# Kernel optimization log

Hardware: AMD Instinct MI355X
Metric: run time of the kernel (lower is better)

Reference implementation:

```python
import jax, jax.numpy as jnp
import numpy as np

ALPHA = 0.1       # args.alpha
T = 1.0           # args.T temperature
SIGMA = 64.0      # Gaussian kernel bandwidth of kernel_function
B_CONST = 1.0     # B in get_lambda
N_ITERS = 50      # 2^-50 << tol=1e-8, matches the break condition of the 1000-iter loop
HW = 256          # image resolution (upsample target)


def _features(feat):
    # get_feature: bilinear upsample (align_corners=False == half-pixel, as jax.image.resize) then sigmoid(x/T)
    n, c, _, _ = feat.shape
    up = jax.image.resize(feat, (n, c, HW, HW), method='bilinear')
    return jax.nn.sigmoid(up / T)


def setup_inputs() -> dict:
    key = jax.random.key(0)
    k1, k2, k3, k4 = jax.random.split(key, 4)
    return {
        'cal_feat': jax.random.normal(k1, (256, 1, 64, 64), jnp.float32),
        'test_feat': jax.random.normal(k2, (32, 1, 64, 64), jnp.float32),
        'cal_gt': jax.random.randint(k3, (256, 1, 256, 256), 0, 2, jnp.int32),
        'test_gt': jax.random.randint(k4, (32, 1, 256, 256), 0, 2, jnp.int32),
    }


def reference(cal_feat, test_feat, cal_gt, test_gt):
    cal_res = _features(cal_feat)    # [N,1,H,W] in (0,1)
    test_res = _features(test_feat)  # [B,1,H,W]
    N = cal_res.shape[0]
    B = test_res.shape[0]
    f32 = cal_res.dtype

    # kernel_function.get_weight: Gaussian RBF on flattened features, plus self-weight 1, row-normalized -> [B, N+1]
    cf = cal_res.reshape(N, -1)
    tf = test_res.reshape(B, -1)
    d2 = (tf * tf).sum(-1)[:, None] + (cf * cf).sum(-1)[None, :] - 2.0 * (tf @ cf.T)
    k = jnp.exp(-d2 / (2.0 * SIGMA * SIGMA))
    w = jnp.concatenate([k, jnp.ones((B, 1), f32)], axis=1)
    w = w / w.sum(axis=1, keepdims=True)

    # FNR_i(t) = #{positive pixels of cal sample i with score < t} / #positives
    # (pred = res >= t, so false negatives are positive pixels with res < t). Precompute sorted
    # positive-pixel scores per cal sample so the bisection is a batched searchsorted.
    gt = (cal_gt > 0).reshape(N, -1)
    pos = jnp.sum(gt, axis=1)                                    # [N]
    scores = jnp.where(gt, cal_res.reshape(N, -1), jnp.inf)
    sorted_scores = jnp.sort(scores, axis=1)                     # [N, HW*HW], padding at +inf
    pos_f = jnp.maximum(pos, 1).astype(f32)

    def fnr_at(t):  # t: [B] thresholds -> [N, B]
        cnt = jax.vmap(lambda s: jnp.searchsorted(s, t, side='left'))(sorted_scores)
        return cnt.astype(f32) / pos_f[:, None]

    # batched bisection on lambda (get_lambda, vectorized over the B test samples)
    def body(carry, _):
        low, high = carry
        lam = 0.5 * (low + high)
        fnr = fnr_at(1.0 - lam)                                   # [N, B]
        risk = jnp.einsum('bn,nb->b', w[:, :-1], fnr) + w[:, -1] * B_CONST
        high = jnp.where(risk < ALPHA, lam, high)
        low = jnp.where(risk >= ALPHA, lam, low)
        return (low, high), None

    init = (jnp.zeros((B,), f32), jnp.ones((B,), f32))
    (low, _), _ = jax.lax.scan(body, init, None, length=N_ITERS)
    lam = low  # _lambda = low after the loop

    # prediction set, size and per-test FNR (get_fnr_list on the test sample)
    pred = test_res >= (1.0 - lam)[:, None, None, None]           # [B,1,H,W] bool
    size = jnp.sum(pred, axis=(1, 2, 3)).astype(f32)
    tgt = test_gt > 0
    tp = jnp.sum(pred & tgt, axis=(1, 2, 3)).astype(f32)
    tpos = jnp.maximum(jnp.sum(tgt, axis=(1, 2, 3)), 1).astype(f32)
    fnr_test = 1.0 - tp / tpos                                    # fdr_tensor, [B]
    return fnr_test, lam, size
```

## Files before the change

### kernel.cpp

```cpp
#include <hip/hip_runtime.h>


#define NPIX 65536
#define HB 16256
#define CDF_STRIDE 16272
#define ALPHA 0.1f

#define OFF_TESTRES  0
#define OFF_CALBF    8388608u
#define OFF_TESTBF   41943040u
#define OFF_GROUPED  46137344u
#define OFF_CDF      79691776u
#define OFF_GPART    96354304u
#define OFF_CC       98451456u
#define OFF_THR      98452480u
#define OFF_LAM      98452608u
#define OFF_FACC     98452736u

typedef __attribute__((ext_vector_type(8))) short bf16x8;
typedef __attribute__((ext_vector_type(16))) float f32x16;

__device__ __forceinline__ unsigned short f2bf_rne(float f) {
  unsigned u = __float_as_uint(f);
  return (unsigned short)((u + 0x7FFFu + ((u >> 16) & 1u)) >> 16);
}

struct RowIp {
  const float* f;
  int x0, x1;
  float omwx, wx;
  __device__ __forceinline__ float operator()(int j) const {
    return f[j * 64 + x0] * omwx + f[j * 64 + x1] * wx;
  }
};

template<int MCNT, typename RV, typename BODY>
__device__ __forceinline__ void scan_rows(RV rv, bool lowq, float omwy, float wy,
                                          int m0, BODY body) {
  if (lowq) {
    float rP = rv(m0 > 0 ? m0 - 1 : 0);
    #pragma unroll 8
    for (int i = 0; i < MCNT; ++i) {
      float rC = rv(m0 + i);
      float v = rP * omwy + rC * wy;
      body(i, 1.f / (1.f + __expf(-v)));
      rP = rC;
    }
  } else {
    float rC = rv(m0);
    #pragma unroll 8
    for (int i = 0; i < MCNT; ++i) {
      int j = m0 + i + 1;
      if (j > 63) j = 63;
      float rN = rv(j);
      float v = rC * omwy + rN * wy;
      body(i, 1.f / (1.f + __expf(-v)));
      rC = rN;
    }
  }
}

__global__ __launch_bounds__(1024, 4) void k_cal(const float* __restrict__ featc,
                                                 const int* __restrict__ gt,
                                                 unsigned short* __restrict__ calbf,
                                                 unsigned* __restrict__ cdf,
                                                 unsigned short* __restrict__ grouped,
                                                 float* __restrict__ cc,
                                                 const float* __restrict__ featt,
                                                 float* __restrict__ tres,
                                                 unsigned short* __restrict__ tbf) {
  __shared__ unsigned smem[16384];
  __shared__ float ri[16384];
  const int n = blockIdx.x, tid = threadIdx.x;
  const int lane = tid & 63, wv = tid >> 6;
  const int x = tid & 255, yq = tid >> 8;
  for (int i = tid; i < 16320; i += 1024) smem[i] = 0;
  const float* fc = featc + n * 4096;
  for (int flat = tid; flat < 16384; flat += 1024) {
    int m = flat >> 8, xx = flat & 255;
    float sxx = 0.25f * (float)xx - 0.375f;
    int x0f = (int)floorf(sxx);
    float wxx = sxx - (float)x0f;
    int xx1 = x0f + 1;
    int xx0 = x0f < 0 ? 0 : x0f;
    if (xx1 > 63) xx1 = 63;
    ri[flat] = fc[m * 64 + xx0] * (1.f - wxx) + fc[m * 64 + xx1] * wxx;
  }
  const int* gtn = gt + (size_t)n * NPIX;
  unsigned short* cbn = calbf + (size_t)n * NPIX;
  float sx = 0.25f * (float)x - 0.375f;
  int x0 = (int)floorf(sx);
  float wx = sx - (float)x0;
  int x1 = x0 + 1;
  if (x0 < 0) x0 = 0;
  if (x1 > 63) x1 = 63;
  const float wy = (yq == 0) ? 0.625f : (yq == 1) ? 0.875f : (yq == 2) ? 0.125f : 0.375f;
  const float omwy = 1.f - wy;
  const bool lowq = (yq < 2);
  const int pb = (yq << 8) + x;
  __syncthreads();
  const float* rix = ri + x;
  auto rv = [&](int j) { return rix[j << 8]; };
  unsigned long long pm = 0ull;
  float sumsq = 0.f;
  scan_rows<64>(rv, lowq, omwy, wy, 0, [&](int i, float s) {
    int p = (i << 10) + pb;
    unsigned short bh = f2bf_rne(s);
    cbn[p] = bh;
    float sr = __uint_as_float((unsigned)bh << 16);
    sumsq += sr * sr;
    if (gtn[p] > 0) {
      pm |= (1ull << i);
      atomicAdd(&smem[__float_as_uint(s) >> 16], 1u);
    }
  });
  #pragma unroll
  for (int off = 32; off; off >>= 1) sumsq += __shfl_xor(sumsq, off);
  if (lane == 0) smem[16336 + wv] = __float_as_uint(sumsq);
  __syncthreads();
  if (tid == 0) {
    float c = 0.f;
    for (int w = 0; w < 16; ++w) c += __uint_as_float(smem[16336 + w]);
    cc[n] = c;
  }
  unsigned* cdfn = cdf + (size_t)n * CDF_STRIDE;
  if (tid < 256) {
    const int base = tid * 64;
    unsigned psum = 0;
    if (base < HB) {
      for (int j = 0; j < 64; ++j) psum += smem[base + ((j + tid) & 63)];
    }
    unsigned inc = psum;
    #pragma unroll
    for (int off = 1; off < 64; off <<= 1) {
      unsigned v = __shfl_up(inc, off);
      if (lane >= off) inc += v;
    }
    if (lane == 63) smem[16320 + wv] = inc;
  }
  __syncthreads();
  if (tid < 256) {
    const int base = tid * 64;
    unsigned psum = 0;
    if (base < HB) {
      for (int j = 0; j < 64; ++j) psum += smem[base + ((j + tid) & 63)];
    }
    unsigned inc = psum;
    #pragma unroll
    for (int off = 1; off < 64; off <<= 1) {
      unsigned v = __shfl_up(inc, off);
      if (lane >= off) inc += v;
    }
    unsigned woff = 0;
    for (int w = 0; w < wv; ++w) woff += smem[16320 + w];
    unsigned run = woff + inc - psum;
    if (base < HB) {
      for (int j = 0; j < 64; ++j) {
        unsigned h = smem[base + j];
        smem[base + j] = run;
        run += h;
      }
    }
    if (tid == 255) cdfn[HB] = woff + inc;
  }
  __syncthreads();
  for (int i = tid; i < HB; i += 1024) cdfn[i] = smem[i];
  __syncthreads();
  unsigned short* gn = grouped + (size_t)n * NPIX;
  scan_rows<64>(rv, lowq, omwy, wy, 0, [&](int i, float s) {
    if (pm & (1ull << i)) {
      unsigned bits = __float_as_uint(s);
      unsigned idx = atomicAdd(&smem[bits >> 16], 1u);
      gn[idx] = (unsigned short)(bits & 0xFFFFu);
    }
  });
  const int tb2 = n >> 3, m0 = (n & 7) * 8;
  const float* tfp = featt + tb2 * 4096;
  float* resb = tres + (size_t)tb2 * NPIX;
  unsigned short* tbn = tbf + (size_t)tb2 * NPIX;
  const RowIp rvt{tfp, x0, x1, 1.f - wx, wx};
  const int pbt = ((m0 * 4 + yq) << 8) + x;
  scan_rows<8>(rvt, lowq, omwy, wy, m0, [&](int i, float s) {
    int p = pbt + (i << 10);
    resb[p] = s;
    tbn[p] = f2bf_rne(s);
  });
}

__global__ __launch_bounds__(256) void k_gemm(const unsigned short* __restrict__ tbf,
                                              const unsigned short* __restrict__ cbf,
                                              float* __restrict__ gpart) {
  __shared__ __align__(16) unsigned short As[16384];
  __shared__ __align__(16) unsigned short Bs[16384];
  __shared__ float lred[4][1024];
  const int tid = threadIdx.x;
  const int lane = tid & 63, wv = tid >> 6;
  const int r = lane & 31, half = lane >> 5;
  const int nt = blockIdx.x;
  f32x16 acc;
  #pragma unroll
  for (int i = 0; i < 16; ++i) acc[i] = 0.f;
  for (int ch = 0; ch < 2; ++ch) {
    const size_t kbase = (size_t)blockIdx.y * 1024 + ch * 512;
    __syncthreads();
    #pragma unroll
    for (int s = 0; s < 16; ++s) {
      int flat = s * 256 + tid;
      int rem = flat & 2047;
      int row = rem >> 6, kb = rem & 63;
      const unsigned short* src = (flat >= 2048)
          ? cbf + (size_t)(nt * 32 + row) * NPIX + kbase + kb * 8
          : tbf + (size_t)row * NPIX + kbase + kb * 8;
      int slot = ((kb << 5) + row) ^ (kb & 31);
      int4 v = *(const int4*)src;
      *(int4*)((flat >= 2048 ? Bs : As) + slot * 8) = v;
    }
    __syncthreads();
    #pragma unroll
    for (int i = 0; i < 8; ++i) {
      int k8 = (wv << 4) + i * 2 + half;
      int slot = ((k8 << 5) + r) ^ (k8 & 31);
      bf16x8 a = *(const bf16x8*)(As + slot * 8);
      bf16x8 b = *(const bf16x8*)(Bs + slot * 8);
      acc = __builtin_amdgcn_mfma_f32_32x32x16_bf16(a, b, acc, 0, 0, 0);
    }
  }
  #pragma unroll
  for (int rg = 0; rg < 16; ++rg) {
    int m = (rg & 3) + 8 * (rg >> 2) + 4 * half;
    lred[wv][m * 32 + r] = acc[rg];
  }
  __syncthreads();
  float* gp = gpart + (size_t)(blockIdx.y * 8 + nt) * 1024;
  for (int e = tid; e < 1024; e += 256)
    gp[e] = lred[0][e] + lred[1][e] + lred[2][e] + lred[3][e];
}

__global__ __launch_bounds__(512) void k_quant(const float* __restrict__ gpart,
                                               const float* __restrict__ cc,
                                               const unsigned* __restrict__ cdf,
                                               const unsigned short* __restrict__ grouped,
                                               const unsigned short* __restrict__ tbf,
                                               float* __restrict__ lam,
                                               float* __restrict__ thr,
                                               int* __restrict__ facc) {
  __shared__ float qs[256];
  __shared__ float bins[4096];
  __shared__ float red[8];
  __shared__ float bc[4];
  __shared__ unsigned sBin;
  const int b = blockIdx.x, tid = threadIdx.x;
  const int lane = tid & 63, wv = tid >> 6;

  if (tid < 4) facc[b * 4 + tid] = 0;
  for (int i = tid; i < 4096; i += 512) bins[i] = 0.f;
  if (tid == 0) sBin = 0xFFFFFFFFu;

  float ts = 0.f;
  const int4* tbp = (const int4*)(tbf + (size_t)b * NPIX);
  for (int i = tid; i < 8192; i += 512) {
    int4 v = tbp[i];
    unsigned w0 = (unsigned)v.x, w1 = (unsigned)v.y, w2 = (unsigned)v.z, w3 = (unsigned)v.w;
    float f;
    f = __uint_as_float(w0 << 16); ts += f * f;
    f = __uint_as_float(w0 & 0xFFFF0000u); ts += f * f;
    f = __uint_as_float(w1 << 16); ts += f * f;
    f = __uint_as_float(w1 & 0xFFFF0000u); ts += f * f;
    f = __uint_as_float(w2 << 16); ts += f * f;
    f = __uint_as_float(w2 & 0xFFFF0000u); ts += f * f;
    f = __uint_as_float(w3 << 16); ts += f * f;
    f = __uint_as_float(w3 & 0xFFFF0000u); ts += f * f;
  }
  #pragma unroll
  for (int off = 32; off; off >>= 1) ts += __shfl_xor(ts, off);
  if (lane == 0) red[wv] = ts;
  __syncthreads();
  if (tid == 0) {
    float t = 0.f;
    for (int w = 0; w < 8; ++w) t += red[w];
    bc[0] = t;
  }
  __syncthreads();
  const float ttv = bc[0];

  float k = 0.f;
  if (tid < 256) {
    const float* gp = gpart + ((tid >> 5) * 1024) + (b * 32) + (tid & 31);
    float g = 0.f;
    #pragma unroll 8
    for (int ks = 0; ks < 64; ++ks) g += gp[(size_t)ks * 8192];
    float d2 = ttv + cc[tid] - 2.f * g;
    k = expf(-d2 * (1.f / 8192.f));
  }
  float v = k;
  #pragma unroll
  for (int off = 32; off; off >>= 1) v += __shfl_xor(v, off);
  if (lane == 0) red[wv] = v;
  __syncthreads();
  if (tid == 0) {
    float ws = 1.f;
    for (int w = 0; w < 8; ++w) ws += red[w];
    bc[1] = ws;
  }
  __syncthreads();
  const float wsum = bc[1];
  const float wlast = 1.f / wsum;
  const float R = ALPHA - wlast;
  if (R <= 0.f) {
    if (tid == 0) { lam[b] = 1.0f; thr[b] = 0.0f; }
    return;
  }
  if (tid < 256) {
    unsigned pos = cdf[(size_t)tid * CDF_STRIDE + HB];
    qs[tid] = k / (wsum * (float)(pos ? pos : 1u));
  }
  __syncthreads();

  int lo = 0, hi = HB;
  float baseS = 0.f;
  for (int it = 0; it < 14; ++it) {
    int mid = (lo + hi) >> 1;
    float p = 0.f;
    if (tid < 256) p = qs[tid] * (float)cdf[(size_t)tid * CDF_STRIDE + mid];
    float r = p;
    #pragma unroll
    for (int off = 32; off; off >>= 1) r += __shfl_xor(r, off);
    if (lane == 0) red[wv] = r;
    __syncthreads();
    if (tid == 0) {
      float s = 0.f;
      for (int w = 0; w < 8; ++w) s += red[w];
      bc[2] = s;
    }
    __syncthreads();
    float S = bc[2];
    if (S < R) { lo = mid; baseS = S; } else { hi = mid; }
  }
  const int B = lo;

  {
    const int n = tid >> 1;
    const float q = qs[n];
    const unsigned* cn = cdf + (size_t)n * CDF_STRIDE;
    const unsigned short* gn = grouped + (size_t)n * NPIX;
    unsigned e0 = cn[B + 1];
    for (unsigned j = cn[B] + (tid & 1); j < e0; j += 2)
      atomicAdd(&bins[gn[j] >> 4], q);
  }
  __syncthreads();

  if (wv == 0) {
    float s = 0.f;
    for (int j = 0; j < 64; ++j) s += bins[lane * 64 + j];
    float inc = s;
    #pragma unroll
    for (int off = 1; off < 64; off <<= 1) {
      float u = __shfl_up(inc, off);
      if (lane >= off) inc += u;
    }
    float pre = inc - s;
    bool hit = (baseS + pre < R) && (baseS + inc >= R);
    unsigned long long m = __ballot(hit);
    int ow = m ? (__ffsll((unsigned long long)m) - 1) : -1;
    if (lane == ow) {
      float run = baseS + pre;
      unsigned bin = (unsigned)lane * 64 + 63;
      for (int j = 0; j < 64; ++j) {
        float bv = bins[lane * 64 + j];
        if (run + bv >= R) { bin = (unsigned)lane * 64 + j; break; }
        run += bv;
      }
      sBin = bin;
    }
    if (m == 0 && lane == 0) sBin = 4095u;
  }
  __syncthreads();
  if (tid == 0) {
    unsigned tb = ((unsigned)B << 16) | (sBin << 4);
    lam[b] = 1.0f - __uint_as_float(tb | 0x8u);
    thr[b] = __uint_as_float((tb | 0xFu) + 1u);
  }
}

__global__ __launch_bounds__(256) void k_finalp(const float* __restrict__ tres,
                                                const int* __restrict__ tgt,
                                                const float* __restrict__ thr,
                                                const float* __restrict__ lam,
                                                int* __restrict__ facc,
                                                float* __restrict__ out) {
  __shared__ int red[12];
  const int b = blockIdx.x, seg = blockIdx.y, tid = threadIdx.x;
  const int lane = tid & 63, wv = tid >> 6;
  const float th = thr[b];
  const float* rb = tres + (size_t)b * NPIX + seg * 8192;
  const int* gb = tgt + (size_t)b * NPIX + seg * 8192;
  int sz = 0, tp = 0, tpos = 0;
  for (int i = 0; i < 32; ++i) {
    int p = i * 256 + tid;
    int pred = (rb[p] >= th) ? 1 : 0;
    int tg = (gb[p] > 0) ? 1 : 0;
    sz += pred;
    tp += pred & tg;
    tpos += tg;
  }
  #pragma unroll
  for (int off = 32; off; off >>= 1) {
    sz += __shfl_xor(sz, off);
    tp += __shfl_xor(tp, off);
    tpos += __shfl_xor(tpos, off);
  }
  if (lane == 0) { red[wv] = sz; red[4 + wv] = tp; red[8 + wv] = tpos; }
  __syncthreads();
  if (tid == 0) {
    int s0 = red[0] + red[1] + red[2] + red[3];
    int s1 = red[4] + red[5] + red[6] + red[7];
    int s2 = red[8] + red[9] + red[10] + red[11];
    atomicAdd(&facc[b * 4 + 0], s0);
    atomicAdd(&facc[b * 4 + 1], s1);
    atomicAdd(&facc[b * 4 + 2], s2);
    __threadfence();
    int old = atomicAdd(&facc[b * 4 + 3], 1);
    if (old == 7) {
      int fsz = atomicAdd(&facc[b * 4 + 0], 0);
      int ftp = atomicAdd(&facc[b * 4 + 1], 0);
      int ftpos = atomicAdd(&facc[b * 4 + 2], 0);
      float tposf = (float)(ftpos > 0 ? ftpos : 1);
      out[b] = 1.f - (float)ftp / tposf;
      out[32 + b] = lam[b];
      out[64 + b] = (float)fsz;
    }
  }
}

extern "C" void kernel_launch(void* const* d_in, const int* in_sizes, int n_in,
                              void* d_out, int out_size, void* d_ws, size_t ws_size,
                              hipStream_t stream) {
  const float* cal_feat = (const float*)d_in[0];
  const float* test_feat = (const float*)d_in[1];
  const int* cal_gt = (const int*)d_in[2];
  const int* test_gt = (const int*)d_in[3];
  float* out = (float*)d_out;
  char* ws = (char*)d_ws;

  float* test_res = (float*)(ws + OFF_TESTRES);
  unsigned short* cal_bf = (unsigned short*)(ws + OFF_CALBF);
  unsigned short* test_bf = (unsigned short*)(ws + OFF_TESTBF);
  unsigned short* grouped = (unsigned short*)(ws + OFF_GROUPED);
  unsigned* cdf = (unsigned*)(ws + OFF_CDF);
  float* gpart = (float*)(ws + OFF_GPART);
  float* cc = (float*)(ws + OFF_CC);
  float* thr = (float*)(ws + OFF_THR);
  float* lam = (float*)(ws + OFF_LAM);
  int* facc = (int*)(ws + OFF_FACC);

  k_cal<<<dim3(256), dim3(1024), 0, stream>>>(cal_feat, cal_gt, cal_bf, cdf, grouped, cc,
                                              test_feat, test_res, test_bf);
  k_gemm<<<dim3(8, 64), dim3(256), 0, stream>>>(test_bf, cal_bf, gpart);
  k_quant<<<dim3(32), dim3(512), 0, stream>>>(gpart, cc, cdf, grouped, test_bf, lam, thr, facc);
  k_finalp<<<dim3(32, 8), dim3(256), 0, stream>>>(test_res, test_gt, thr, lam, facc, out);
}
```

Baseline: 251.2 us.

## Fuse final prediction-set reduction into quantile kernel and vectorize bin scatter

New measurement: 254.4 us. No clear change (+1.3%).

```diff
diff --git a/kernel.cpp b/kernel.cpp
--- a/kernel.cpp
+++ b/kernel.cpp
@@ -13,9 +13,6 @@
 #define OFF_CDF      79691776u
 #define OFF_GPART    96354304u
 #define OFF_CC       98451456u
-#define OFF_THR      98452480u
-#define OFF_LAM      98452608u
-#define OFF_FACC     98452736u
 
 typedef __attribute__((ext_vector_type(8))) short bf16x8;
 typedef __attribute__((ext_vector_type(16))) float f32x16;
@@ -241,18 +238,18 @@
                                                const unsigned* __restrict__ cdf,
                                                const unsigned short* __restrict__ grouped,
                                                const unsigned short* __restrict__ tbf,
-                                               float* __restrict__ lam,
-                                               float* __restrict__ thr,
-                                               int* __restrict__ facc) {
+                                               const float* __restrict__ tres,
+                                               const int* __restrict__ tgt,
+                                               float* __restrict__ out) {
   __shared__ float qs[256];
   __shared__ float bins[4096];
   __shared__ float red[8];
   __shared__ float bc[4];
   __shared__ unsigned sBin;
+  __shared__ int ired[24];
   const int b = blockIdx.x, tid = threadIdx.x;
   const int lane = tid & 63, wv = tid >> 6;
 
-  if (tid < 4) facc[b * 4 + tid] = 0;
   for (int i = tid; i < 4096; i += 512) bins[i] = 0.f;
   if (tid == 0) sBin = 0xFFFFFFFFu;
 
@@ -300,108 +297,113 @@
   if (tid == 0) {
     float ws = 1.f;
     for (int w = 0; w < 8; ++w) ws += red[w];
-    bc[1] = ws;
-  }
-  __syncthreads();
-  const float wsum = bc[1];
-  const float wlast = 1.f / wsum;
-  const float R = ALPHA - wlast;
-  if (R <= 0.f) {
-    if (tid == 0) { lam[b] = 1.0f; thr[b] = 0.0f; }
-    return;
-  }
-  if (tid < 256) {
-    unsigned pos = cdf[(size_t)tid * CDF_STRIDE + HB];
-    qs[tid] = k / (wsum * (float)(pos ? pos : 1u));
-  }
-  __syncthreads();
-
-  int lo = 0, hi = HB;
-  float baseS = 0.f;
-  for (int it = 0; it < 14; ++it) {
-    int mid = (lo + hi) >> 1;
-    float p = 0.f;
-    if (tid < 256) p = qs[tid] * (float)cdf[(size_t)tid * CDF_STRIDE + mid];
-    float r = p;
-    #pragma unroll
-    for (int off = 32; off; off >>= 1) r += __shfl_xor(r, off);
-    if (lane == 0) red[wv] = r;
+    bc[0] = ws;
+  }
+  __syncthreads();
+  const float wsum = bc[0];
+  const float R = ALPHA - 1.f / wsum;
+
+  if (R > 0.f) {
+    if (tid < 256) {
+      unsigned pos = cdf[(size_t)tid * CDF_STRIDE + HB];
+      qs[tid] = k / (wsum * (float)(pos ? pos : 1u));
+    }
+    __syncthreads();
+    int lo = 0, hi = HB;
+    float baseS = 0.f;
+    for (int it = 0; it < 14; ++it) {
+      int mid = (lo + hi) >> 1;
+      float p = 0.f;
+      if (tid < 256) p = qs[tid] * (float)cdf[(size_t)tid * CDF_STRIDE + mid];
+      float r = p;
+      #pragma unroll
+      for (int off = 32; off; off >>= 1) r += __shfl_xor(r, off);
+      if (lane == 0) red[wv] = r;
+      __syncthreads();
+      if (tid == 0) {
+        float s = 0.f;
+        for (int w = 0; w < 8; ++w) s += red[w];
+        bc[1] = s;
+      }
+      __syncthreads();
+      float S = bc[1];
+      if (S < R) { lo = mid; baseS = S; } else { hi = mid; }
+    }
+    const int B = lo;
+
+    {
+      const int n = tid >> 1;
+      const float q = qs[n];
+      const unsigned* cn = cdf + (size_t)n * CDF_STRIDE;
+      const unsigned short* gn = grouped + (size_t)n * NPIX;
+      unsigned s0 = cn[B], e0 = cn[B + 1];
+      unsigned mid = (s0 + e0) >> 1;
+      unsigned a0 = (tid & 1) ? mid : s0;
+      unsigned a1 = (tid & 1) ? e0 : mid;
+      while (a0 < a1 && (a0 & 7u)) { atomicAdd(&bins[gn[a0] >> 4], q); ++a0; }
+      for (; a0 + 8 <= a1; a0 += 8) {
+        int4 vv = *(const int4*)(gn + a0);
+        unsigned u0 = (unsigned)vv.x, u1 = (unsigned)vv.y, u2 = (unsigned)vv.z, u3 = (unsigned)vv.w;
+        atomicAdd(&bins[(u0 & 0xFFFFu) >> 4], q);
+        atomicAdd(&bins[u0 >> 20], q);
+        atomicAdd(&bins[(u1 & 0xFFFFu) >> 4], q);
+        atomicAdd(&bins[u1 >> 20], q);
+        atomicAdd(&bins[(u2 & 0xFFFFu) >> 4], q);
+        atomicAdd(&bins[u2 >> 20], q);
+        atomicAdd(&bins[(u3 & 0xFFFFu) >> 4], q);
+        atomicAdd(&bins[u3 >> 20], q);
+      }
+      for (; a0 < a1; ++a0) atomicAdd(&bins[gn[a0] >> 4], q);
+    }
+    __syncthreads();
+
+    if (wv == 0) {
+      float s = 0.f;
+      for (int j = 0; j < 64; ++j) s += bins[lane * 64 + j];
+      float inc = s;
+      #pragma unroll
+      for (int off = 1; off < 64; off <<= 1) {
+        float u = __shfl_up(inc, off);
+        if (lane >= off) inc += u;
+      }
+      float pre = inc - s;
+      bool hit = (baseS + pre < R) && (baseS + inc >= R);
+      unsigned long long m = __ballot(hit);
+      int ow = m ? (__ffsll((unsigned long long)m) - 1) : -1;
+      if (lane == ow) {
+        float run = baseS + pre;
+        unsigned bin = (unsigned)lane * 64 + 63;
+        for (int j = 0; j < 64; ++j) {
+          float bv = bins[lane * 64 + j];
+          if (run + bv >= R) { bin = (unsigned)lane * 64 + j; break; }
+          run += bv;
+        }
+        sBin = bin;
+      }
+      if (m == 0 && lane == 0) sBin = 4095u;
+    }
     __syncthreads();
     if (tid == 0) {
-      float s = 0.f;
-      for (int w = 0; w < 8; ++w) s += red[w];
-      bc[2] = s;
-    }
-    __syncthreads();
-    float S = bc[2];
-    if (S < R) { lo = mid; baseS = S; } else { hi = mid; }
-  }
-  const int B = lo;
-
-  {
-    const int n = tid >> 1;
-    const float q = qs[n];
-    const unsigned* cn = cdf + (size_t)n * CDF_STRIDE;
-    const unsigned short* gn = grouped + (size_t)n * NPIX;
-    unsigned e0 = cn[B + 1];
-    for (unsigned j = cn[B] + (tid & 1); j < e0; j += 2)
-      atomicAdd(&bins[gn[j] >> 4], q);
-  }
-  __syncthreads();
-
-  if (wv == 0) {
-    float s = 0.f;
-    for (int j = 0; j < 64; ++j) s += bins[lane * 64 + j];
-    float inc = s;
-    #pragma unroll
-    for (int off = 1; off < 64; off <<= 1) {
-      float u = __shfl_up(inc, off);
-      if (lane >= off) inc += u;
-    }
-    float pre = inc - s;
-    bool hit = (baseS + pre < R) && (baseS + inc >= R);
-    unsigned long long m = __ballot(hit);
-    int ow = m ? (__ffsll((unsigned long long)m) - 1) : -1;
-    if (lane == ow) {
-      float run = baseS + pre;
-      unsigned bin = (unsigned)lane * 64 + 63;
-      for (int j = 0; j < 64; ++j) {
-        float bv = bins[lane * 64 + j];
-        if (run + bv >= R) { bin = (unsigned)lane * 64 + j; break; }
-        run += bv;
-      }
-      sBin = bin;
-    }
-    if (m == 0 && lane == 0) sBin = 4095u;
-  }
-  __syncthreads();
-  if (tid == 0) {
-    unsigned tb = ((unsigned)B << 16) | (sBin << 4);
-    lam[b] = 1.0f - __uint_as_float(tb | 0x8u);
-    thr[b] = __uint_as_float((tb | 0xFu) + 1u);
-  }
-}
-
-__global__ __launch_bounds__(256) void k_finalp(const float* __restrict__ tres,
-                                                const int* __restrict__ tgt,
-                                                const float* __restrict__ thr,
-                                                const float* __restrict__ lam,
-                                                int* __restrict__ facc,
-                                                float* __restrict__ out) {
-  __shared__ int red[12];
-  const int b = blockIdx.x, seg = blockIdx.y, tid = threadIdx.x;
-  const int lane = tid & 63, wv = tid >> 6;
-  const float th = thr[b];
-  const float* rb = tres + (size_t)b * NPIX + seg * 8192;
-  const int* gb = tgt + (size_t)b * NPIX + seg * 8192;
+      unsigned tb = ((unsigned)B << 16) | (sBin << 4);
+      bc[2] = 1.0f - __uint_as_float(tb | 0x8u);
+      bc[3] = __uint_as_float((tb | 0xFu) + 1u);
+    }
+    __syncthreads();
+  }
+  const float lamv = (R > 0.f) ? bc[2] : 1.0f;
+  const float th = (R > 0.f) ? bc[3] : 0.0f;
+
+  const float4* rb4 = (const float4*)(tres + (size_t)b * NPIX);
+  const int4* gb4 = (const int4*)(tgt + (size_t)b * NPIX);
   int sz = 0, tp = 0, tpos = 0;
-  for (int i = 0; i < 32; ++i) {
-    int p = i * 256 + tid;
-    int pred = (rb[p] >= th) ? 1 : 0;
-    int tg = (gb[p] > 0) ? 1 : 0;
-    sz += pred;
-    tp += pred & tg;
-    tpos += tg;
+  for (int i = tid; i < 16384; i += 512) {
+    float4 rr = rb4[i];
+    int4 gg = gb4[i];
+    int p0 = rr.x >= th, p1 = rr.y >= th, p2 = rr.z >= th, p3 = rr.w >= th;
+    int t0 = gg.x > 0, t1 = gg.y > 0, t2 = gg.z > 0, t3 = gg.w > 0;
+    sz += p0 + p1 + p2 + p3;
+    tp += (p0 & t0) + (p1 & t1) + (p2 & t2) + (p3 & t3);
+    tpos += t0 + t1 + t2 + t3;
   }
   #pragma unroll
   for (int off = 32; off; off >>= 1) {
@@ -409,26 +411,15 @@
     tp += __shfl_xor(tp, off);
     tpos += __shfl_xor(tpos, off);
   }
-  if (lane == 0) { red[wv] = sz; red[4 + wv] = tp; red[8 + wv] = tpos; }
+  if (lane == 0) { ired[wv] = sz; ired[8 + wv] = tp; ired[16 + wv] = tpos; }
   __syncthreads();
   if (tid == 0) {
-    int s0 = red[0] + red[1] + red[2] + red[3];
-    int s1 = red[4] + red[5] + red[6] + red[7];
-    int s2 = red[8] + red[9] + red[10] + red[11];
-    atomicAdd(&facc[b * 4 + 0], s0);
-    atomicAdd(&facc[b * 4 + 1], s1);
-    atomicAdd(&facc[b * 4 + 2], s2);
-    __threadfence();
-    int old = atomicAdd(&facc[b * 4 + 3], 1);
-    if (old == 7) {
-      int fsz = atomicAdd(&facc[b * 4 + 0], 0);
-      int ftp = atomicAdd(&facc[b * 4 + 1], 0);
-      int ftpos = atomicAdd(&facc[b * 4 + 2], 0);
-      float tposf = (float)(ftpos > 0 ? ftpos : 1);
-      out[b] = 1.f - (float)ftp / tposf;
-      out[32 + b] = lam[b];
-      out[64 + b] = (float)fsz;
-    }
+    int s0 = 0, s1 = 0, s2 = 0;
+    for (int w = 0; w < 8; ++w) { s0 += ired[w]; s1 += ired[8 + w]; s2 += ired[16 + w]; }
+    float tposf = (float)(s2 > 0 ? s2 : 1);
+    out[b] = 1.f - (float)s1 / tposf;
+    out[32 + b] = lamv;
+    out[64 + b] = (float)s0;
   }
 }
 
@@ -449,13 +440,10 @@
   unsigned* cdf = (unsigned*)(ws + OFF_CDF);
   float* gpart = (float*)(ws + OFF_GPART);
   float* cc = (float*)(ws + OFF_CC);
-  float* thr = (float*)(ws + OFF_THR);
-  float* lam = (float*)(ws + OFF_LAM);
-  int* facc = (int*)(ws + OFF_FACC);
 
   k_cal<<<dim3(256), dim3(1024), 0, stream>>>(cal_feat, cal_gt, cal_bf, cdf, grouped, cc,
                                               test_feat, test_res, test_bf);
   k_gemm<<<dim3(8, 64), dim3(256), 0, stream>>>(test_bf, cal_bf, gpart);
-  k_quant<<<dim3(32), dim3(512), 0, stream>>>(gpart, cc, cdf, grouped, test_bf, lam, thr, facc);
-  k_finalp<<<dim3(32, 8), dim3(256), 0, stream>>>(test_res, test_gt, thr, lam, facc, out);
-}
+  k_quant<<<dim3(32), dim3(512), 0, stream>>>(gpart, cc, cdf, grouped, test_bf,
+                                              test_res, test_gt, out);
+}
```
